# Kernel tuning notes

Measured on AMD Instinct MI355X. Metric: run time of the kernel, lower is better.

## Reference

```python
import jax, jax.numpy as jnp
import numpy as np

N_SAMPLES = 32768
WINDOW = 2048
HOP = WINDOW // 2
N_FRAMES = N_SAMPLES // HOP  # 32 resonance frames
BASE_RES = 0.5
RES_SPAN = 1.0 - BASE_RES
RES_FACTOR = 0.9
N_RES = 32
EXPR = 4
CPD = 16
N_COEFFS = WINDOW // 2 + 1  # 1025


def interpolate_last_axis(x, new_size):
    # linear interpolation along last axis (align_corners=False semantics)
    old = x.shape[-1]
    pos = (jnp.arange(new_size, dtype=jnp.float32) + 0.5) * (old / new_size) - 0.5
    pos = jnp.clip(pos, 0.0, old - 1.0)
    lo = jnp.floor(pos).astype(jnp.int32)
    hi = jnp.minimum(lo + 1, old - 1)
    w = pos - lo.astype(jnp.float32)
    return x[..., lo] * (1.0 - w) + x[..., hi] * w


def overlap_add(frames):
    # frames: (..., n_frames, window); hop = window//2; output (..., n_frames*hop)
    *lead, nf, w = frames.shape
    hop = w // 2
    a = frames[..., :hop]
    b = frames[..., hop:]
    b = jnp.concatenate([jnp.zeros_like(b[..., :1, :]), b[..., :-1, :]], axis=-2)
    return (a + b).reshape(*lead, nf * hop)


def freq_domain_transfer_function_to_resonance(window_size, decay_coeffs, n_frames, start_phase, start_mags):
    # decay_coeffs/start_phase/start_mags: (nr, expr, n_coeffs); log-space decay scan
    log_decay = jnp.log(decay_coeffs + 1e-12)[..., None, :]  # (nr, expr, 1, nc)
    shape = log_decay.shape[:-2] + (n_frames, log_decay.shape[-1])
    cum = jnp.cumsum(jnp.broadcast_to(log_decay, shape), axis=-2)  # decay^(f+1)
    mags = jnp.exp(cum) * start_mags[..., None, :]
    spec = mags * jnp.exp(1j * start_phase[..., None, :])
    frames = jnp.fft.irfft(spec, n=window_size, axis=-1)  # (nr, expr, n_frames, window)
    t = jnp.arange(window_size, dtype=jnp.float32)
    hann = 0.5 - 0.5 * jnp.cos(2.0 * jnp.pi * t / window_size)
    return overlap_add(frames * hann)  # (nr, expr, n_frames*hop)


def unit_norm(x):
    return x / (jnp.linalg.norm(x, axis=-1, keepdims=True) + 1e-8)


def fft_convolve(a, b):
    n = a.shape[-1]
    fa = jnp.fft.rfft(a, n=2 * n, axis=-1)
    fb = jnp.fft.rfft(b, n=2 * n, axis=-1)
    return jnp.fft.irfft(fa * fb, n=2 * n, axis=-1)[..., :n]


def setup_inputs() -> dict:
    key = jax.random.key(0)
    ks = jax.random.split(key, 10)
    control_signal = jax.random.normal(ks[0], (2, 4, CPD, 128), dtype=jnp.float32)
    deformations = jax.random.normal(ks[1], (2, 4, EXPR, 128), dtype=jnp.float32) * 0.1
    router = jax.random.uniform(ks[2], (CPD, N_RES), minval=-1.0, maxval=1.0)

    def init_resonance(k):
        k1, k2 = jax.random.split(k)
        res = jax.random.uniform(k1, (N_RES, N_COEFFS, 1), minval=0.01, maxval=1.0)
        deform = jax.random.uniform(k2, (1, N_COEFFS, EXPR), minval=-0.02, maxval=0.02)
        return res + deform

    amp = init_resonance(ks[3])
    phase = init_resonance(ks[4])
    decay = init_resonance(ks[5])
    gains = jax.random.uniform(ks[6], (N_RES, 1), minval=0.01, maxval=1.1)
    return {"control_signal": control_signal, "deformations": deformations,
            "router": router, "amp": amp, "phase": phase, "decay": decay, "gains": gains}


def reference(control_signal, deformations, router, amp, phase, decay, gains):
    b, e, cpd, frames = control_signal.shape
    nr = router.shape[1]
    # route control plane -> resonances: (b,e,nr,frames)
    routed = jnp.einsum('becf,cr->berf', control_signal, router)
    before_upsample = routed
    # (nr, n_coeffs, expr) -> (nr, expr, n_coeffs)
    amp_t = jnp.transpose(amp, (0, 2, 1))
    phase_t = jnp.transpose(phase, (0, 2, 1))
    decay_t = jnp.transpose(decay, (0, 2, 1))
    d_coeffs = BASE_RES + jax.nn.sigmoid(decay_t) * RES_SPAN * RES_FACTOR
    res = freq_domain_transfer_function_to_resonance(
        WINDOW, d_coeffs, N_FRAMES, jnp.tanh(phase_t) * jnp.pi, jnp.abs(amp_t))
    res = unit_norm(res)[None, None]  # (1,1,nr,expr,N)
    routed_up = interpolate_last_axis(routed[:, :, :, None, :], N_SAMPLES)  # (b,e,nr,1,N)
    noise = jax.random.uniform(jax.random.key(123), routed_up.shape, minval=-1.0, maxval=1.0)
    routed_up = routed_up * noise
    conv = fft_convolve(routed_up, res)  # (b,e,nr,expr,N)
    d = deformations.at[:, :, 0, :].add(1.0)  # base deformation favors first expressivity
    d = jax.nn.softmax(d, axis=2)[:, :, None, :, :]  # (b,e,1,expr,def_frames)
    d = interpolate_last_axis(d, N_SAMPLES)
    x = jnp.sum(d * conv, axis=-2)  # mix over expressivity -> (b,e,nr,N)
    summed = jnp.tanh(x * jnp.abs(gains).reshape(1, 1, nr, 1))
    summed = jnp.sum(summed, axis=-2, keepdims=True)  # (b,e,1,N)
    return summed, before_upsample
```

## Files before the change

### kernel.cpp

```cpp
#include <hip/hip_runtime.h>
#include <hip/hip_fp16.h>
#include <stdint.h>


#define PI_F     3.14159265358979323846f
#define TWOPI_F  6.28318530717958647692f
#define UNIT64K  (TWOPI_F/65536.0f)
#define UNIT2K   (TWOPI_F/2048.0f)
#define SCALE64K (1.0f/65536.0f)
#define SKP(i)   ((i) + 4*((i) >> 4))
#define RPW 328

__device__ __forceinline__ float2 cmul(float2 a, float2 b){
  return make_float2(a.x*b.x - a.y*b.y, a.x*b.y + a.y*b.x);
}

__device__ __forceinline__ float2 twid(uint32_t e, float unit, float sign){
  float ang = (float)e * unit;
  float sn, cn;
  __sincosf(ang, &sn, &cn);
  return make_float2(cn, sign*sn);
}

__device__ __forceinline__ uint32_t rotl32(uint32_t v, int r){
  return (v << r) | (v >> (32 - r));
}

__device__ __forceinline__ void threefry2x32(uint32_t c0, uint32_t c1,
                                             uint32_t& o0, uint32_t& o1){
  const uint32_t k0 = 0u, k1 = 123u;
  const uint32_t k2 = 0x1BD11BDAu ^ k0 ^ k1;
  const uint32_t ks[3] = {k0, k1, k2};
  uint32_t x0 = c0 + k0, x1 = c1 + k1;
#pragma unroll
  for (int i = 0; i < 5; i++){
    if ((i & 1) == 0){
      x0 += x1; x1 = rotl32(x1,13); x1 ^= x0;
      x0 += x1; x1 = rotl32(x1,15); x1 ^= x0;
      x0 += x1; x1 = rotl32(x1,26); x1 ^= x0;
      x0 += x1; x1 = rotl32(x1, 6); x1 ^= x0;
    } else {
      x0 += x1; x1 = rotl32(x1,17); x1 ^= x0;
      x0 += x1; x1 = rotl32(x1,29); x1 ^= x0;
      x0 += x1; x1 = rotl32(x1,16); x1 ^= x0;
      x0 += x1; x1 = rotl32(x1,24); x1 ^= x0;
    }
    x0 += ks[(i+1)%3];
    x1 += ks[(i+2)%3] + (uint32_t)(i+1);
  }
  o0 = x0; o1 = x1;
}

__device__ __forceinline__ float jax_noise(uint32_t p){
  uint32_t b0, b1;
  threefry2x32(0u, p, b0, b1);
  uint32_t bits = b0 ^ b1;
  float u = __uint_as_float((bits >> 9) | 0x3f800000u) - 1.0f;
  return fmaxf(-1.0f, u*2.0f - 1.0f);
}

__device__ __forceinline__ void interp128(int t, int& lo, int& hi, float& w){
  float posf = ((float)t + 0.5f) * (1.0f/256.0f) - 0.5f;
  posf = fminf(fmaxf(posf, 0.0f), 127.0f);
  lo = (int)posf;
  hi = lo + 1; if (hi > 127) hi = 127;
  w = posf - (float)lo;
}

__device__ __forceinline__ __half2 u2h(uint32_t u){
  union { uint32_t u; __half2 h; } x; x.u = u; return x.h;
}
__device__ __forceinline__ uint32_t h2u(__half2 h){
  union { uint32_t u; __half2 h; } x; x.h = h; return x.u;
}
__device__ __forceinline__ constexpr int sw4(int k){ return ((k & 3) << 2) | (k >> 2); }
__device__ __forceinline__ constexpr int br4(int x){
  return ((x & 1) << 3) | ((x & 2) << 1) | ((x & 4) >> 1) | ((x & 8) >> 3);
}

__device__ __forceinline__ void cws(float2& u, const float c, const float s){
  const float x = u.x*c - u.y*s;
  u.y = u.x*s + u.y*c;
  u.x = x;
}
__device__ __forceinline__ void cwv(float2& u, const float2 w){
  const float x = u.x*w.x - u.y*w.y;
  u.y = u.x*w.y + u.y*w.x;
  u.x = x;
}

__device__ __forceinline__ void dft4(float2& a, float2& b, float2& c, float2& d,
                                     const float sgn){
  float2 t0 = make_float2(a.x + c.x, a.y + c.y);
  float2 t1 = make_float2(a.x - c.x, a.y - c.y);
  float2 t2 = make_float2(b.x + d.x, b.y + d.y);
  float2 t3 = make_float2(b.x - d.x, b.y - d.y);
  float2 i3 = make_float2(-sgn*t3.y, sgn*t3.x);
  a = make_float2(t0.x + t2.x, t0.y + t2.y);
  c = make_float2(t0.x - t2.x, t0.y - t2.y);
  b = make_float2(t1.x + i3.x, t1.y + i3.y);
  d = make_float2(t1.x - i3.x, t1.y - i3.y);
}

#define DFT16_TW(d, sgn) do { \
  const float C1_ = 0.92387953251128674f, S1_ = 0.38268343236508978f; \
  const float C2_ = 0.70710678118654752f; \
  cws(d[5],  C1_,  (sgn)*S1_); \
  cws(d[6],  C2_,  (sgn)*C2_); \
  cws(d[7],  S1_,  (sgn)*C1_); \
  cws(d[9],  C2_,  (sgn)*C2_); \
  cws(d[10], 0.0f, (sgn)); \
  cws(d[11], -C2_, (sgn)*C2_); \
  cws(d[13], S1_,  (sgn)*C1_); \
  cws(d[14], -C2_, (sgn)*C2_); \
  cws(d[15], -C1_, -(sgn)*S1_); \
} while(0)

__device__ __forceinline__ void dft16(float2* d, const float sgn){
#pragma unroll
  for (int nb = 0; nb < 4; nb++) dft4(d[nb], d[nb+4], d[nb+8], d[nb+12], sgn);
  DFT16_TW(d, sgn);
#pragma unroll
  for (int ka = 0; ka < 4; ka++) dft4(d[4*ka], d[4*ka+1], d[4*ka+2], d[4*ka+3], sgn);
}
__device__ __forceinline__ void dft16b(float2* d, const float sgn){
#pragma unroll
  for (int nb = 0; nb < 4; nb++) dft4(d[4*nb], d[4*nb+1], d[4*nb+2], d[4*nb+3], sgn);
  DFT16_TW(d, sgn);
#pragma unroll
  for (int ka = 0; ka < 4; ka++) dft4(d[ka], d[ka+4], d[ka+8], d[ka+12], sgn);
}

__device__ __forceinline__ void pass1_fwd(__half2* buf, const float2* twl, const int t){
  const int row = t >> 4, L = t & 15;
  __half2* BR = buf + row*RPW;
  float2 d[16];
#pragma unroll
  for (int H = 0; H < 16; H++) d[H] = __half22float2(BR[L + 20*H]);
  dft16(d, -1.0f);
#pragma unroll
  for (int k1 = 0; k1 < 16; k1++){
    float2 y = d[sw4(k1)];
    cwv(y, twl[(L*k1) & 255]);
    BR[L + 20*k1] = __floats2half2_rn(y.x, y.y);
  }
}

__global__ void k_routed(const float* __restrict__ ctrl, const float* __restrict__ defm,
                         const float* __restrict__ router,
                         float* __restrict__ w_routed, float* __restrict__ w_sm,
                         float* __restrict__ out1){
  int idx = blockIdx.x*blockDim.x + threadIdx.x;
  if (idx < 32768){
    int f = idx & 127, r = (idx >> 7) & 31, be = idx >> 12;
    float acc = 0.0f;
#pragma unroll
    for (int c = 0; c < 16; c++)
      acc += ctrl[(be*16 + c)*128 + f] * router[c*32 + r];
    w_routed[idx] = acc;
    out1[idx] = acc;
  } else if (idx < 32768 + 1024){
    int j = idx - 32768;
    int f = j & 127, be = j >> 7;
    float v[4];
#pragma unroll
    for (int x = 0; x < 4; x++)
      v[x] = defm[(be*4 + x)*128 + f] + (x == 0 ? 1.0f : 0.0f);
    float mx = fmaxf(fmaxf(v[0], v[1]), fmaxf(v[2], v[3]));
    float s = 0.0f;
#pragma unroll
    for (int x = 0; x < 4; x++){ v[x] = expf(v[x] - mx); s += v[x]; }
#pragma unroll
    for (int x = 0; x < 4; x++) w_sm[(be*4 + x)*128 + f] = v[x]/s;
  }
}

__global__ void k_prep(const float* __restrict__ amp, const float* __restrict__ phase,
                       const float* __restrict__ decay, float4* __restrict__ pql){
  const int idx = blockIdx.x*256 + threadIdx.x;
  if (idx >= 131200) return;
  float a  = fabsf(amp[idx]);
  float ph = tanhf(phase[idx]) * PI_F;
  float sg = 1.0f / (1.0f + expf(-decay[idx]));
  float dc = 0.5f + 0.45f * sg;
  float L  = logf(dc + 1e-12f);
  float sn, cs;
  sincosf(ph, &sn, &cs);
  pql[idx] = make_float4(a*cs, a*sn, L, 0.0f);
}

__global__ void k_frames(const float4* __restrict__ pql, float2* __restrict__ w_fr){
  const int wg = blockIdx.x;
  const int f = wg & 31;
  const int rp = wg >> 5;
  const int p = rp & 1;
  const int r = rp >> 1;
  const int t = threadIdx.x;
  __shared__ float2 buf[2048];
  __shared__ float2 twl2[1024];

  for (int i = t; i < 1024; i += 256)
    twl2[i] = twid((uint32_t)i, UNIT2K, +1.0f);

  const float fp1 = (float)(f + 1);
  for (int k = t; k <= 1024; k += 256){
    float2 S[2];
#pragma unroll
    for (int d = 0; d < 2; d++){
      const int x = 2*p + d;
      const float4 q = pql[(r*1025 + k)*4 + x];
      const float e = __expf(q.z * fp1);
      float re = e*q.x, im = e*q.y;
      if (k == 0 || k == 1024) im = 0.0f;
      S[d] = make_float2(re, im);
    }
    buf[__brev((uint32_t)k) >> 21] =
        make_float2(S[0].x - S[1].y, S[0].y + S[1].x);
    if (k >= 1 && k <= 1023)
      buf[__brev((uint32_t)(2048 - k)) >> 21] =
          make_float2(S[0].x + S[1].y, -S[0].y + S[1].x);
  }
  __syncthreads();
  for (int s = 10; s >= 0; s--){
    const int ls = 10 - s;
    const int hl = 1 << ls;
    for (int bi = t; bi < 1024; bi += 256){
      const int g = bi >> ls, j = bi & (hl - 1);
      const int i0 = g*2*hl + j, i1 = i0 + hl;
      float2 pp = buf[i0], qq = buf[i1];
      float2 w = twl2[j << s];
      float2 v = cmul(qq, w);
      buf[i0] = make_float2(pp.x+v.x, pp.y+v.y);
      buf[i1] = make_float2(pp.x-v.x, pp.y-v.y);
    }
    __syncthreads();
  }
  float2* O = w_fr + (size_t)wg*2048;
  for (int u = t; u < 2048; u += 256){
    float hann = 0.5f - 0.5f*cosf(TWOPI_F * (float)u / 2048.0f);
    float sc = (1.0f/2048.0f) * hann;
    O[u] = make_float2(buf[u].x*sc, buf[u].y*sc);
  }
}

__global__ void k_ola(const float2* __restrict__ w_fr, float* __restrict__ w_resT,
                      float* __restrict__ w_sumsq){
  const int wg = blockIdx.x;
  const int cq = wg & 7;
  const int rp = wg >> 3;
  const int c0 = cq*32;
  const int r = rp >> 1, p = rp & 1;
  const int ch0 = r*4 + p*2;
  const int t = threadIdx.x;
  __shared__ float tx[32][129], ty[32][129];
  __shared__ float red[2][256];
  const float2* F = w_fr + (size_t)rp*32*2048;
  float acc0 = 0.0f, acc1 = 0.0f;
#pragma unroll
  for (int it = 0; it < 16; it++){
    const int idx = it*256 + t;
    const int cp = idx & 31, m = idx >> 5;
    const int n = c0 + cp + 256*m;
    const int f = n >> 10, u = n & 1023;
    float2 a = F[(size_t)f*2048 + u];
    float vx = a.x, vy = a.y;
    if (f > 0){
      float2 b = F[(size_t)(f-1)*2048 + u + 1024];
      vx += b.x; vy += b.y;
    }
    tx[cp][m] = vx; ty[cp][m] = vy;
    acc0 += vx*vx; acc1 += vy*vy;
  }
  red[0][t] = acc0; red[1][t] = acc1;
  __syncthreads();
#pragma unroll
  for (int it = 0; it < 16; it++){
    const int idx = it*256 + t;
    const int m = idx & 127, cp = idx >> 7;
    w_resT[(size_t)ch0*32768 + (size_t)(c0+cp)*128 + m]     = tx[cp][m];
    w_resT[(size_t)(ch0+1)*32768 + (size_t)(c0+cp)*128 + m] = ty[cp][m];
  }
  for (int off = 128; off > 0; off >>= 1){
    __syncthreads();
    if (t < off){ red[0][t] += red[0][t+off]; red[1][t] += red[1][t+off]; }
  }
  if (t == 0){
    atomicAdd(&w_sumsq[ch0],     red[0][0]);
    atomicAdd(&w_sumsq[ch0 + 1], red[1][0]);
  }
}

__global__ void k_norm(const float* __restrict__ w_sumsq, float* __restrict__ w_invnorm){
  const int s = threadIdx.x;
  if (s < 128) w_invnorm[s] = 1.0f/(sqrtf(w_sumsq[s]) + 1e-8f);
}

__global__ __launch_bounds__(256, 4)
void k_fwdA(const int mode, const float* __restrict__ w_resT,
            const float* __restrict__ w_invnorm,
            const float* __restrict__ w_routed,
            __half2* __restrict__ outh){
  const int wg = blockIdx.x;
  const int cq = wg & 15;
  const int sig = wg >> 4;
  const int t = threadIdx.x;
  const int cc = t >> 4;
  const int c  = cq*16 + cc;
  __shared__ alignas(16) __half2 buf[16*RPW];

  {
    const int mL = t & 15;
    float2 d[16];
    if (mode == 0){
      const int rr = sig >> 1, pq = sig & 1;
      const int ch0 = rr*4 + pq*2;
      const float inv0 = w_invnorm[ch0], inv1 = w_invnorm[ch0+1];
      const float* X0 = w_resT + (size_t)ch0*32768 + (size_t)c*128;
      const float* X1 = w_resT + (size_t)(ch0+1)*32768 + (size_t)c*128;
#pragma unroll
      for (int mH = 0; mH < 8; mH++){
        const int m = mL + 16*mH;
        d[mH] = make_float2(X0[m]*inv0, X1[m]*inv1);
      }
#pragma unroll
      for (int mH = 8; mH < 16; mH++) d[mH] = make_float2(0.0f, 0.0f);
    } else {
      const float* rp = w_routed + sig*128;
#pragma unroll
      for (int mH = 0; mH < 8; mH++){
        const int m = mL + 16*mH;
        const int n = c + 256*m;
        int lo, hi; float w;
        interp128(n, lo, hi, w);
        float rv = rp[lo]*(1.0f - w) + rp[hi]*w;
        d[mH] = make_float2(rv * jax_noise((uint32_t)sig*32768u + (uint32_t)n), 0.0f);
      }
#pragma unroll
      for (int mH = 8; mH < 16; mH++) d[mH] = make_float2(0.0f, 0.0f);
    }
    dft16(d, -1.0f);
    const float2 wstep = twid((uint32_t)(c + 256*mL) & 0xFFFFu, UNIT64K, -1.0f);
    float2 w = wstep;
    __half2* BR = buf + cc*RPW;
    BR[mL] = __floats2half2_rn(d[0].x, d[0].y);
#pragma unroll
    for (int rl = 1; rl < 16; rl++){
      float2 y = d[sw4(rl)];
      cwv(y, w);
      w = cmul(w, wstep);
      BR[20*rl + mL] = __floats2half2_rn(y.x, y.y);
    }
  }
  __syncthreads();
  {
    const int rl = t & 15;
    const __half2* BG = buf + cc*RPW + 20*rl;
    float2 v[16];
#pragma unroll
    for (int q4 = 0; q4 < 4; q4++){
      const uint4 ld = *reinterpret_cast<const uint4*>(BG + 4*q4);
      v[4*q4+0] = __half22float2(u2h(ld.x));
      v[4*q4+1] = __half22float2(u2h(ld.y));
      v[4*q4+2] = __half22float2(u2h(ld.z));
      v[4*q4+3] = __half22float2(u2h(ld.w));
    }
    dft16(v, -1.0f);
    const float2 wstep = twid((uint32_t)(16*c) & 0xFFFFu, UNIT64K, -1.0f);
    float2 w = wstep;
    __half2 y[16];
    y[0] = __floats2half2_rn(v[0].x, v[0].y);
#pragma unroll
    for (int rh = 1; rh < 16; rh++){
      float2 u = v[sw4(rh)];
      cwv(u, w);
      w = cmul(w, wstep);
      y[rh] = __floats2half2_rn(u.x, u.y);
    }
    uint4* O4 = reinterpret_cast<uint4*>(
        outh + (size_t)sig*65536 + (size_t)c*256 + 16*br4(rl));
#pragma unroll
    for (int q4 = 0; q4 < 4; q4++){
      uint4 st;
      st.x = h2u(y[br4(4*q4+0)]);
      st.y = h2u(y[br4(4*q4+1)]);
      st.z = h2u(y[br4(4*q4+2)]);
      st.w = h2u(y[br4(4*q4+3)]);
      O4[q4] = st;
    }
  }
}

__global__ __launch_bounds__(256, 4)
void k_fwdB(const __half2* __restrict__ spech, __half2* __restrict__ resp_t){
  const int wg = blockIdx.x;
  const int mq = wg & 15;
  const int sig = wg >> 4;
  const int m16 = mq*16;
  const int t = threadIdx.x;
  __shared__ alignas(16) __half2 buf[16*RPW];
  __shared__ float2 twl[256];
  twl[t] = twid((uint32_t)t << 8, UNIT64K, -1.0f);
  const __half2* base = spech + (size_t)sig*65536;
  {
    const int mm = t & 15, q = t >> 4;
    __half2* BR = buf + mm*RPW;
#pragma unroll
    for (int i = 0; i < 16; i++)
      BR[20*i + q] = base[(size_t)(16*i + q)*256 + m16 + mm];
  }
  __syncthreads();
  pass1_fwd(buf, twl, t);
  __syncthreads();
  {
    const int k1 = t >> 4, row = t & 15;
    __half2* BG = buf + row*RPW + 20*k1;
    float2 v[16];
#pragma unroll
    for (int cc = 0; cc < 4; cc++){
      const uint4 ld = *reinterpret_cast<const uint4*>(BG + 4*cc);
      v[4*cc+0] = __half22float2(u2h(ld.x));
      v[4*cc+1] = __half22float2(u2h(ld.y));
      v[4*cc+2] = __half22float2(u2h(ld.z));
      v[4*cc+3] = __half22float2(u2h(ld.w));
    }
    dft16(v, -1.0f);
    uint4* O4 = reinterpret_cast<uint4*>(resp_t + (((size_t)sig*16 + mq)*256 + t)*16);
#pragma unroll
    for (int cc = 0; cc < 4; cc++){
      uint4 st;
      st.x = h2u(__floats2half2_rn(v[4*cc+0].x, v[4*cc+0].y));
      st.y = h2u(__floats2half2_rn(v[4*cc+1].x, v[4*cc+1].y));
      st.z = h2u(__floats2half2_rn(v[4*cc+2].x, v[4*cc+2].y));
      st.w = h2u(__floats2half2_rn(v[4*cc+3].x, v[4*cc+3].y));
      O4[cc] = st;
    }
  }
}

__global__ __launch_bounds__(256, 4)
void k_conv(const __half2* __restrict__ ruspec,
            const __half2* __restrict__ resp_t,
            __half2* __restrict__ chunkbuf, const int gbase){
  const int wg = blockIdx.x;
  const int mq = wg & 15;
  const int p  = (wg >> 4) & 1;
  const int gl = wg >> 5;
  const int g = gbase + gl;
  const int r = g & 31;
  const int m16 = mq*16;
  const int t = threadIdx.x;
  __shared__ alignas(16) __half2 buf[16*RPW];
  __shared__ float2 twl[256];
  twl[t] = twid((uint32_t)t << 8, UNIT64K, -1.0f);

  {
    const uint4* A4 = reinterpret_cast<const uint4*>(
        ruspec + (size_t)g*65536 + (size_t)t*256 + m16);
    uint4 a0 = A4[0], a1 = A4[1], a2 = A4[2], a3 = A4[3];
    const int cs = SKP(t);
    uint32_t w[16];
    w[0]=a0.x; w[1]=a0.y; w[2]=a0.z; w[3]=a0.w;
    w[4]=a1.x; w[5]=a1.y; w[6]=a1.z; w[7]=a1.w;
    w[8]=a2.x; w[9]=a2.y; w[10]=a2.z; w[11]=a2.w;
    w[12]=a3.x; w[13]=a3.y; w[14]=a3.z; w[15]=a3.w;
#pragma unroll
    for (int mm = 0; mm < 16; mm++)
      buf[mm*RPW + cs] = u2h(w[mm]);
  }
  __syncthreads();
  pass1_fwd(buf, twl, t);
  __syncthreads();
  {
    const int k1 = t >> 4, row = t & 15;
    __half2* BG = buf + row*RPW + 20*k1;
    float2 v[16];
#pragma unroll
    for (int cc = 0; cc < 4; cc++){
      const uint4 ld = *reinterpret_cast<const uint4*>(BG + 4*cc);
      v[4*cc+0] = __half22float2(u2h(ld.x));
      v[4*cc+1] = __half22float2(u2h(ld.y));
      v[4*cc+2] = __half22float2(u2h(ld.z));
      v[4*cc+3] = __half22float2(u2h(ld.w));
    }
    const uint4* Bt = reinterpret_cast<const uint4*>(
        resp_t + (((size_t)(r*2 + p)*16 + mq)*256 + t)*16);
    uint4 b0 = Bt[0], b1 = Bt[1], b2 = Bt[2], b3 = Bt[3];
    dft16(v, -1.0f);
    uint32_t bw[16];
    bw[0]=b0.x; bw[1]=b0.y; bw[2]=b0.z; bw[3]=b0.w;
    bw[4]=b1.x; bw[5]=b1.y; bw[6]=b1.z; bw[7]=b1.w;
    bw[8]=b2.x; bw[9]=b2.y; bw[10]=b2.z; bw[11]=b2.w;
    bw[12]=b3.x; bw[13]=b3.y; bw[14]=b3.z; bw[15]=b3.w;
#pragma unroll
    for (int pp = 0; pp < 16; pp++){
      const float2 b = __half22float2(u2h(bw[pp]));
      const float zx = v[pp].x, zy = v[pp].y;
      v[pp] = make_float2((zx*b.x - zy*b.y)*SCALE64K,
                          (zx*b.y + zy*b.x)*SCALE64K);
    }
    dft16b(v, +1.0f);
    __half2 h[16];
#pragma unroll
    for (int n2 = 0; n2 < 16; n2++){
      float2 m = v[n2];
      const float2 w = twl[(n2*k1) & 255];
      const float x = m.x*w.x + m.y*w.y;
      m.y = -m.x*w.y + m.y*w.x;
      m.x = x;
      h[n2] = __floats2half2_rn(m.x, m.y);
    }
#pragma unroll
    for (int cc = 0; cc < 4; cc++){
      uint4 st;
      st.x = h2u(h[4*cc+0]);
      st.y = h2u(h[4*cc+1]);
      st.z = h2u(h[4*cc+2]);
      st.w = h2u(h[4*cc+3]);
      *reinterpret_cast<uint4*>(BG + 4*cc) = st;
    }
  }
  __syncthreads();
  {
    const int row = t >> 4, L = t & 15;
    __half2* BR = buf + row*RPW;
    float2 d[16];
#pragma unroll
    for (int k1 = 0; k1 < 16; k1++) d[k1] = __half22float2(BR[L + 20*k1]);
    dft16(d, +1.0f);
#pragma unroll
    for (int H = 0; H < 16; H++){
      const float2 x = d[sw4(H)];
      BR[L + 20*H] = __floats2half2_rn(x.x, x.y);
    }
  }
  __syncthreads();
  {
    uint4* O4 = reinterpret_cast<uint4*>(
        chunkbuf + (size_t)(gl*2 + p)*65536 + (size_t)t*256 + m16);
    const int cs = SKP(t);
#pragma unroll
    for (int q4 = 0; q4 < 4; q4++){
      uint4 st;
      st.x = h2u(buf[(4*q4+0)*RPW + cs]);
      st.y = h2u(buf[(4*q4+1)*RPW + cs]);
      st.z = h2u(buf[(4*q4+2)*RPW + cs]);
      st.w = h2u(buf[(4*q4+3)*RPW + cs]);
      O4[q4] = st;
    }
  }
}

__global__ __launch_bounds__(256, 4)
void k_invA_w(const __half2* __restrict__ chunkbuf, const int gbase,
              const float* __restrict__ w_sm, const float* __restrict__ gains,
              float* __restrict__ out0){
  const int wg = blockIdx.x;
  const int c8 = wg & 31;
  const int gl = wg >> 5;
  const int g = gbase + gl;
  const int r = g & 31, be = g >> 5;
  const int c0 = c8*8;
  const int t = threadIdx.x;
  __shared__ alignas(16) __half2 buf[16*RPW];
  __shared__ float sm_lds[512];
  sm_lds[t]       = w_sm[be*512 + t];
  sm_lds[256 + t] = w_sm[be*512 + 256 + t];

  const int row = t >> 4;
  const int p   = row >> 3;
  const int cc  = row & 7;
  const int c   = c0 + cc;
  {
    const int u = t & 15;
    const uint4* C4 = reinterpret_cast<const uint4*>(
        chunkbuf + (size_t)(gl*2 + p)*65536 + (size_t)c*256 + 16*br4(u));
    uint4 z0 = C4[0], z1 = C4[1], z2 = C4[2], z3 = C4[3];
    uint32_t zw[16];
    zw[0]=z0.x; zw[1]=z0.y; zw[2]=z0.z; zw[3]=z0.w;
    zw[4]=z1.x; zw[5]=z1.y; zw[6]=z1.z; zw[7]=z1.w;
    zw[8]=z2.x; zw[9]=z2.y; zw[10]=z2.z; zw[11]=z2.w;
    zw[12]=z3.x; zw[13]=z3.y; zw[14]=z3.z; zw[15]=z3.w;
    const float2 wstep = twid((uint32_t)(16*c) & 0xFFFFu, UNIT64K, +1.0f);
    float2 w = make_float2(1.0f, 0.0f);
    float2 d[16];
#pragma unroll
    for (int rh = 0; rh < 16; rh++){
      d[rh] = cmul(__half22float2(u2h(zw[br4(rh)])), w);
      w = cmul(w, wstep);
    }
    dft16(d, +1.0f);
    __half2* BR = buf + row*RPW;
#pragma unroll
    for (int mL = 0; mL < 16; mL++){
      const float2 s = d[sw4(mL)];
      BR[20*mL + u] = __floats2half2_rn(s.x, s.y);
    }
  }
  __syncthreads();
  const int mL = t & 15;
  float2 v[16];
  {
    const __half2* BG = buf + row*RPW + 20*mL;
#pragma unroll
    for (int q4 = 0; q4 < 4; q4++){
      const uint4 ld = *reinterpret_cast<const uint4*>(BG + 4*q4);
      v[4*q4+0] = __half22float2(u2h(ld.x));
      v[4*q4+1] = __half22float2(u2h(ld.y));
      v[4*q4+2] = __half22float2(u2h(ld.z));
      v[4*q4+3] = __half22float2(u2h(ld.w));
    }
  }
  __syncthreads();
  {
    const float2 wstep = twid((uint32_t)(c + 256*mL) & 0xFFFFu, UNIT64K, +1.0f);
    float2 w = wstep;
#pragma unroll
    for (int kL2 = 1; kL2 < 16; kL2++){
      v[kL2] = cmul(v[kL2], w);
      w = cmul(w, wstep);
    }
    dft16(v, +1.0f);
    __half2* BR = buf + row*RPW;
#pragma unroll
    for (int mH = 0; mH < 8; mH++){
      const float2 x = v[sw4(mH)];
      BR[mL + 20*mH] = __floats2half2_rn(x.x, x.y);
    }
  }
  __syncthreads();
  const float gv = fabsf(gains[r]);
#pragma unroll
  for (int it = 0; it < 4; it++){
    const int li = t + it*256;
    const int cc2 = li & 7, m = li >> 3;
    const int tt = c0 + cc2 + 256*m;
    int lo, hi; float w;
    interp128(tt, lo, hi, w);
    const int cell = (m & 15) + 20*(m >> 4);
    float2 z0 = __half22float2(buf[cc2*RPW + cell]);
    float2 z1 = __half22float2(buf[(8 + cc2)*RPW + cell]);
    float dw0 = sm_lds[0*128 + lo]*(1.0f - w) + sm_lds[0*128 + hi]*w;
    float dw1 = sm_lds[1*128 + lo]*(1.0f - w) + sm_lds[1*128 + hi]*w;
    float dw2 = sm_lds[2*128 + lo]*(1.0f - w) + sm_lds[2*128 + hi]*w;
    float dw3 = sm_lds[3*128 + lo]*(1.0f - w) + sm_lds[3*128 + hi]*w;
    float val = dw0*z0.x + dw1*z0.y + dw2*z1.x + dw3*z1.y;
    atomicAdd(&out0[(size_t)be*32768 + tt], tanhf(val*gv));
  }
}

extern "C" void kernel_launch(void* const* d_in, const int* in_sizes, int n_in,
                              void* d_out, int out_size, void* d_ws, size_t ws_size,
                              hipStream_t stream){
  const float* ctrl   = (const float*)d_in[0];
  const float* defm   = (const float*)d_in[1];
  const float* router = (const float*)d_in[2];
  const float* amp    = (const float*)d_in[3];
  const float* phase  = (const float*)d_in[4];
  const float* decay  = (const float*)d_in[5];
  const float* gains  = (const float*)d_in[6];
  float* out = (float*)d_out;
  float* ws  = (float*)d_ws;

  float*   w_resT    = ws;
  float*   w_routed  = ws + 4194304;
  float*   w_sm      = ws + 4227072;
  float*   w_invnorm = ws + 4231168;
  float*   w_sumsq   = ws + 4231296;
  __half2* ruspec_h  = (__half2*)(ws + 4231424);
  __half2* resp_h    = (__half2*)(ws + 21008640);
  __half2* chunk_h   = (__half2*)(ws + 25202944);
  const size_t base_f = 25202944;
  float2* w_fr       = (float2*)ruspec_h;
  __half2* resp_t    = (__half2*)w_resT;
  float4*  pql       = (float4*)resp_h;

  int G = 0;
  for (int gg = 256; gg >= 1; gg >>= 1){
    size_t need = (base_f + (size_t)gg*131072) * sizeof(float);
    if (need <= ws_size){ G = gg; break; }
  }

  hipMemsetAsync(d_out, 0, 262144*sizeof(float), stream);
  k_routed<<<132, 256, 0, stream>>>(ctrl, defm, router, w_routed, w_sm, out + 262144);
  if (G == 0) return;

  hipMemsetAsync(w_sumsq, 0, 128*sizeof(float), stream);
  k_prep<<<513, 256, 0, stream>>>(amp, phase, decay, pql);
  k_frames<<<2048, 256, 0, stream>>>(pql, w_fr);
  k_ola<<<512, 256, 0, stream>>>(w_fr, w_resT, w_sumsq);
  k_norm<<<1, 128, 0, stream>>>(w_sumsq, w_invnorm);
  k_fwdA<<<64*16, 256, 0, stream>>>(0, w_resT, w_invnorm, w_routed, resp_h);
  k_fwdB<<<64*16, 256, 0, stream>>>(resp_h, resp_t);
  k_fwdA<<<256*16, 256, 0, stream>>>(1, w_resT, w_invnorm, w_routed, ruspec_h);
  for (int gb = 0; gb < 256; gb += G){
    k_conv<<<G*32, 256, 0, stream>>>(ruspec_h, resp_t, chunk_h, gb);
    k_invA_w<<<G*32, 256, 0, stream>>>(chunk_h, gb, w_sm, gains, out);
  }
}
```

Measured before the change: 334.0 us.

## Hoist routed-signal forward FFT pass out of conv into separate kernel

The second forward FFT stage of the routed spectrum was recomputed in k_conv once for each of the two p halves. A new k_ruB kernel now computes it once per signal into a new workspace buffer, and k_conv reads the result directly before the pointwise multiply. The shared-memory twiddle table in k_conv is replaced by a per-thread recurrence of complex multiplies. This costs an extra 64 MB-scale workspace buffer, an extra global round trip, and possibly a smaller G batch if the workspace is limited; the twiddle recurrence also adds some rounding error.

```diff
diff --git a/kernel.cpp b/kernel.cpp
--- a/kernel.cpp
+++ b/kernel.cpp
@@ -438,7 +438,60 @@
 }
 
 __global__ __launch_bounds__(256, 4)
-void k_conv(const __half2* __restrict__ ruspec,
+void k_ruB(const __half2* __restrict__ ruspec, __half2* __restrict__ ruf){
+  const int wg = blockIdx.x;
+  const int mq = wg & 15;
+  const int g = wg >> 4;
+  const int m16 = mq*16;
+  const int t = threadIdx.x;
+  __shared__ alignas(16) __half2 buf[16*RPW];
+  __shared__ float2 twl[256];
+  twl[t] = twid((uint32_t)t << 8, UNIT64K, -1.0f);
+  {
+    const uint4* A4 = reinterpret_cast<const uint4*>(
+        ruspec + (size_t)g*65536 + (size_t)t*256 + m16);
+    uint4 a0 = A4[0], a1 = A4[1], a2 = A4[2], a3 = A4[3];
+    const int cs = SKP(t);
+    uint32_t w[16];
+    w[0]=a0.x; w[1]=a0.y; w[2]=a0.z; w[3]=a0.w;
+    w[4]=a1.x; w[5]=a1.y; w[6]=a1.z; w[7]=a1.w;
+    w[8]=a2.x; w[9]=a2.y; w[10]=a2.z; w[11]=a2.w;
+    w[12]=a3.x; w[13]=a3.y; w[14]=a3.z; w[15]=a3.w;
+#pragma unroll
+    for (int mm = 0; mm < 16; mm++)
+      buf[mm*RPW + cs] = u2h(w[mm]);
+  }
+  __syncthreads();
+  pass1_fwd(buf, twl, t);
+  __syncthreads();
+  {
+    const int k1 = t >> 4, row = t & 15;
+    __half2* BG = buf + row*RPW + 20*k1;
+    float2 v[16];
+#pragma unroll
+    for (int cc = 0; cc < 4; cc++){
+      const uint4 ld = *reinterpret_cast<const uint4*>(BG + 4*cc);
+      v[4*cc+0] = __half22float2(u2h(ld.x));
+      v[4*cc+1] = __half22float2(u2h(ld.y));
+      v[4*cc+2] = __half22float2(u2h(ld.z));
+      v[4*cc+3] = __half22float2(u2h(ld.w));
+    }
+    dft16(v, -1.0f);
+    uint4* O4 = reinterpret_cast<uint4*>(ruf + (((size_t)g*16 + mq)*256 + t)*16);
+#pragma unroll
+    for (int cc = 0; cc < 4; cc++){
+      uint4 st;
+      st.x = h2u(__floats2half2_rn(v[4*cc+0].x, v[4*cc+0].y));
+      st.y = h2u(__floats2half2_rn(v[4*cc+1].x, v[4*cc+1].y));
+      st.z = h2u(__floats2half2_rn(v[4*cc+2].x, v[4*cc+2].y));
+      st.w = h2u(__floats2half2_rn(v[4*cc+3].x, v[4*cc+3].y));
+      O4[cc] = st;
+    }
+  }
+}
+
+__global__ __launch_bounds__(256, 4)
+void k_conv(const __half2* __restrict__ ruf,
             const __half2* __restrict__ resp_t,
             __half2* __restrict__ chunkbuf, const int gbase){
   const int wg = blockIdx.x;
@@ -450,65 +503,44 @@
   const int m16 = mq*16;
   const int t = threadIdx.x;
   __shared__ alignas(16) __half2 buf[16*RPW];
-  __shared__ float2 twl[256];
-  twl[t] = twid((uint32_t)t << 8, UNIT64K, -1.0f);
-
-  {
-    const uint4* A4 = reinterpret_cast<const uint4*>(
-        ruspec + (size_t)g*65536 + (size_t)t*256 + m16);
-    uint4 a0 = A4[0], a1 = A4[1], a2 = A4[2], a3 = A4[3];
-    const int cs = SKP(t);
-    uint32_t w[16];
-    w[0]=a0.x; w[1]=a0.y; w[2]=a0.z; w[3]=a0.w;
-    w[4]=a1.x; w[5]=a1.y; w[6]=a1.z; w[7]=a1.w;
-    w[8]=a2.x; w[9]=a2.y; w[10]=a2.z; w[11]=a2.w;
-    w[12]=a3.x; w[13]=a3.y; w[14]=a3.z; w[15]=a3.w;
-#pragma unroll
-    for (int mm = 0; mm < 16; mm++)
-      buf[mm*RPW + cs] = u2h(w[mm]);
-  }
-  __syncthreads();
-  pass1_fwd(buf, twl, t);
-  __syncthreads();
-  {
-    const int k1 = t >> 4, row = t & 15;
-    __half2* BG = buf + row*RPW + 20*k1;
-    float2 v[16];
-#pragma unroll
-    for (int cc = 0; cc < 4; cc++){
-      const uint4 ld = *reinterpret_cast<const uint4*>(BG + 4*cc);
-      v[4*cc+0] = __half22float2(u2h(ld.x));
-      v[4*cc+1] = __half22float2(u2h(ld.y));
-      v[4*cc+2] = __half22float2(u2h(ld.z));
-      v[4*cc+3] = __half22float2(u2h(ld.w));
-    }
+
+  const int k1 = t >> 4, row = t & 15;
+  {
+    const uint4* Zt = reinterpret_cast<const uint4*>(
+        ruf + (((size_t)g*16 + mq)*256 + t)*16);
+    uint4 a0 = Zt[0], a1 = Zt[1], a2 = Zt[2], a3 = Zt[3];
     const uint4* Bt = reinterpret_cast<const uint4*>(
         resp_t + (((size_t)(r*2 + p)*16 + mq)*256 + t)*16);
     uint4 b0 = Bt[0], b1 = Bt[1], b2 = Bt[2], b3 = Bt[3];
-    dft16(v, -1.0f);
-    uint32_t bw[16];
+    uint32_t zw[16], bw[16];
+    zw[0]=a0.x; zw[1]=a0.y; zw[2]=a0.z; zw[3]=a0.w;
+    zw[4]=a1.x; zw[5]=a1.y; zw[6]=a1.z; zw[7]=a1.w;
+    zw[8]=a2.x; zw[9]=a2.y; zw[10]=a2.z; zw[11]=a2.w;
+    zw[12]=a3.x; zw[13]=a3.y; zw[14]=a3.z; zw[15]=a3.w;
     bw[0]=b0.x; bw[1]=b0.y; bw[2]=b0.z; bw[3]=b0.w;
     bw[4]=b1.x; bw[5]=b1.y; bw[6]=b1.z; bw[7]=b1.w;
     bw[8]=b2.x; bw[9]=b2.y; bw[10]=b2.z; bw[11]=b2.w;
     bw[12]=b3.x; bw[13]=b3.y; bw[14]=b3.z; bw[15]=b3.w;
+    float2 v[16];
 #pragma unroll
     for (int pp = 0; pp < 16; pp++){
+      const float2 z = __half22float2(u2h(zw[pp]));
       const float2 b = __half22float2(u2h(bw[pp]));
-      const float zx = v[pp].x, zy = v[pp].y;
-      v[pp] = make_float2((zx*b.x - zy*b.y)*SCALE64K,
-                          (zx*b.y + zy*b.x)*SCALE64K);
+      v[pp] = make_float2((z.x*b.x - z.y*b.y)*SCALE64K,
+                          (z.x*b.y + z.y*b.x)*SCALE64K);
     }
     dft16b(v, +1.0f);
+    const float2 wstep = twid((uint32_t)k1 << 8, UNIT64K, +1.0f);
+    float2 w = wstep;
     __half2 h[16];
-#pragma unroll
-    for (int n2 = 0; n2 < 16; n2++){
-      float2 m = v[n2];
-      const float2 w = twl[(n2*k1) & 255];
-      const float x = m.x*w.x + m.y*w.y;
-      m.y = -m.x*w.y + m.y*w.x;
-      m.x = x;
+    h[0] = __floats2half2_rn(v[0].x, v[0].y);
+#pragma unroll
+    for (int n2 = 1; n2 < 16; n2++){
+      float2 m = cmul(v[n2], w);
+      w = cmul(w, wstep);
       h[n2] = __floats2half2_rn(m.x, m.y);
     }
+    __half2* BG = buf + row*RPW + 20*k1;
 #pragma unroll
     for (int cc = 0; cc < 4; cc++){
       uint4 st;
@@ -521,11 +553,11 @@
   }
   __syncthreads();
   {
-    const int row = t >> 4, L = t & 15;
-    __half2* BR = buf + row*RPW;
+    const int rw = t >> 4, L = t & 15;
+    __half2* BR = buf + rw*RPW;
     float2 d[16];
 #pragma unroll
-    for (int k1 = 0; k1 < 16; k1++) d[k1] = __half22float2(BR[L + 20*k1]);
+    for (int kk = 0; kk < 16; kk++) d[kk] = __half22float2(BR[L + 20*kk]);
     dft16(d, +1.0f);
 #pragma unroll
     for (int H = 0; H < 16; H++){
@@ -668,8 +700,9 @@
   float*   w_sumsq   = ws + 4231296;
   __half2* ruspec_h  = (__half2*)(ws + 4231424);
   __half2* resp_h    = (__half2*)(ws + 21008640);
-  __half2* chunk_h   = (__half2*)(ws + 25202944);
-  const size_t base_f = 25202944;
+  __half2* ruf_h     = (__half2*)(ws + 25202944);
+  __half2* chunk_h   = (__half2*)(ws + 41980160);
+  const size_t base_f = 41980160;
   float2* w_fr       = (float2*)ruspec_h;
   __half2* resp_t    = (__half2*)w_resT;
   float4*  pql       = (float4*)resp_h;
@@ -692,8 +725,9 @@
   k_fwdA<<<64*16, 256, 0, stream>>>(0, w_resT, w_invnorm, w_routed, resp_h);
   k_fwdB<<<64*16, 256, 0, stream>>>(resp_h, resp_t);
   k_fwdA<<<256*16, 256, 0, stream>>>(1, w_resT, w_invnorm, w_routed, ruspec_h);
+  k_ruB<<<256*16, 256, 0, stream>>>(ruspec_h, ruf_h);
   for (int gb = 0; gb < 256; gb += G){
-    k_conv<<<G*32, 256, 0, stream>>>(ruspec_h, resp_t, chunk_h, gb);
+    k_conv<<<G*32, 256, 0, stream>>>(ruf_h, resp_t, chunk_h, gb);
     k_invA_w<<<G*32, 256, 0, stream>>>(chunk_h, gb, w_sm, gains, out);
   }
 }
```

New measurement: 356.9 us. +6.8%, slower.

## Share forward FFT across both response halves in k_conv workgroup

Applied to the files above, without the earlier changes.

Each k_conv workgroup now runs the input load, first forward pass and forward DFT16 once, then processes both p=0 and p=1 response halves. The forward spectrum is staged in a new 16KB shared-memory buffer in half precision and reused for the second pointwise multiply and inverse passes. This halves the ruspec reads and the forward FFT work, and launches half as many workgroups. In exchange each workgroup holds more LDS, which can reduce occupancy, and its work is more serialized.

```diff
diff --git a/kernel.cpp b/kernel.cpp
--- a/kernel.cpp
+++ b/kernel.cpp
@@ -443,13 +443,13 @@
             __half2* __restrict__ chunkbuf, const int gbase){
   const int wg = blockIdx.x;
   const int mq = wg & 15;
-  const int p  = (wg >> 4) & 1;
-  const int gl = wg >> 5;
+  const int gl = wg >> 4;
   const int g = gbase + gl;
   const int r = g & 31;
   const int m16 = mq*16;
   const int t = threadIdx.x;
   __shared__ alignas(16) __half2 buf[16*RPW];
+  __shared__ alignas(16) __half2 Fh[4096];
   __shared__ float2 twl[256];
   twl[t] = twid((uint32_t)t << 8, UNIT64K, -1.0f);
 
@@ -470,9 +470,9 @@
   __syncthreads();
   pass1_fwd(buf, twl, t);
   __syncthreads();
-  {
-    const int k1 = t >> 4, row = t & 15;
-    __half2* BG = buf + row*RPW + 20*k1;
+  const int k1 = t >> 4, row = t & 15;
+  __half2* BG = buf + row*RPW + 20*k1;
+  {
     float2 v[16];
 #pragma unroll
     for (int cc = 0; cc < 4; cc++){
@@ -482,10 +482,20 @@
       v[4*cc+2] = __half22float2(u2h(ld.z));
       v[4*cc+3] = __half22float2(u2h(ld.w));
     }
-    const uint4* Bt = reinterpret_cast<const uint4*>(
-        resp_t + (((size_t)(r*2 + p)*16 + mq)*256 + t)*16);
-    uint4 b0 = Bt[0], b1 = Bt[1], b2 = Bt[2], b3 = Bt[3];
+    const uint4* Bt0 = reinterpret_cast<const uint4*>(
+        resp_t + (((size_t)(r*2 + 0)*16 + mq)*256 + t)*16);
+    uint4 b0 = Bt0[0], b1 = Bt0[1], b2 = Bt0[2], b3 = Bt0[3];
     dft16(v, -1.0f);
+    uint4* F4 = reinterpret_cast<uint4*>(Fh + t*16);
+#pragma unroll
+    for (int cc = 0; cc < 4; cc++){
+      uint4 st;
+      st.x = h2u(__floats2half2_rn(v[4*cc+0].x, v[4*cc+0].y));
+      st.y = h2u(__floats2half2_rn(v[4*cc+1].x, v[4*cc+1].y));
+      st.z = h2u(__floats2half2_rn(v[4*cc+2].x, v[4*cc+2].y));
+      st.w = h2u(__floats2half2_rn(v[4*cc+3].x, v[4*cc+3].y));
+      F4[cc] = st;
+    }
     uint32_t bw[16];
     bw[0]=b0.x; bw[1]=b0.y; bw[2]=b0.z; bw[3]=b0.w;
     bw[4]=b1.x; bw[5]=b1.y; bw[6]=b1.z; bw[7]=b1.w;
@@ -521,11 +531,11 @@
   }
   __syncthreads();
   {
-    const int row = t >> 4, L = t & 15;
-    __half2* BR = buf + row*RPW;
+    const int rw = t >> 4, L = t & 15;
+    __half2* BR = buf + rw*RPW;
     float2 d[16];
 #pragma unroll
-    for (int k1 = 0; k1 < 16; k1++) d[k1] = __half22float2(BR[L + 20*k1]);
+    for (int kk = 0; kk < 16; kk++) d[kk] = __half22float2(BR[L + 20*kk]);
     dft16(d, +1.0f);
 #pragma unroll
     for (int H = 0; H < 16; H++){
@@ -536,7 +546,81 @@
   __syncthreads();
   {
     uint4* O4 = reinterpret_cast<uint4*>(
-        chunkbuf + (size_t)(gl*2 + p)*65536 + (size_t)t*256 + m16);
+        chunkbuf + (size_t)(gl*2 + 0)*65536 + (size_t)t*256 + m16);
+    const int cs = SKP(t);
+#pragma unroll
+    for (int q4 = 0; q4 < 4; q4++){
+      uint4 st;
+      st.x = h2u(buf[(4*q4+0)*RPW + cs]);
+      st.y = h2u(buf[(4*q4+1)*RPW + cs]);
+      st.z = h2u(buf[(4*q4+2)*RPW + cs]);
+      st.w = h2u(buf[(4*q4+3)*RPW + cs]);
+      O4[q4] = st;
+    }
+  }
+  __syncthreads();
+  {
+    const uint4* F4 = reinterpret_cast<const uint4*>(Fh + t*16);
+    uint4 a0 = F4[0], a1 = F4[1], a2 = F4[2], a3 = F4[3];
+    const uint4* Bt1 = reinterpret_cast<const uint4*>(
+        resp_t + (((size_t)(r*2 + 1)*16 + mq)*256 + t)*16);
+    uint4 b0 = Bt1[0], b1 = Bt1[1], b2 = Bt1[2], b3 = Bt1[3];
+    uint32_t zw[16], bw[16];
+    zw[0]=a0.x; zw[1]=a0.y; zw[2]=a0.z; zw[3]=a0.w;
+    zw[4]=a1.x; zw[5]=a1.y; zw[6]=a1.z; zw[7]=a1.w;
+    zw[8]=a2.x; zw[9]=a2.y; zw[10]=a2.z; zw[11]=a2.w;
+    zw[12]=a3.x; zw[13]=a3.y; zw[14]=a3.z; zw[15]=a3.w;
+    bw[0]=b0.x; bw[1]=b0.y; bw[2]=b0.z; bw[3]=b0.w;
+    bw[4]=b1.x; bw[5]=b1.y; bw[6]=b1.z; bw[7]=b1.w;
+    bw[8]=b2.x; bw[9]=b2.y; bw[10]=b2.z; bw[11]=b2.w;
+    bw[12]=b3.x; bw[13]=b3.y; bw[14]=b3.z; bw[15]=b3.w;
+    float2 v[16];
+#pragma unroll
+    for (int pp = 0; pp < 16; pp++){
+      const float2 z = __half22float2(u2h(zw[pp]));
+      const float2 b = __half22float2(u2h(bw[pp]));
+      v[pp] = make_float2((z.x*b.x - z.y*b.y)*SCALE64K,
+                          (z.x*b.y + z.y*b.x)*SCALE64K);
+    }
+    dft16b(v, +1.0f);
+    __half2 h[16];
+#pragma unroll
+    for (int n2 = 0; n2 < 16; n2++){
+      float2 m = v[n2];
+      const float2 w = twl[(n2*k1) & 255];
+      const float x = m.x*w.x + m.y*w.y;
+      m.y = -m.x*w.y + m.y*w.x;
+      m.x = x;
+      h[n2] = __floats2half2_rn(m.x, m.y);
+    }
+#pragma unroll
+    for (int cc = 0; cc < 4; cc++){
+      uint4 st;
+      st.x = h2u(h[4*cc+0]);
+      st.y = h2u(h[4*cc+1]);
+      st.z = h2u(h[4*cc+2]);
+      st.w = h2u(h[4*cc+3]);
+      *reinterpret_cast<uint4*>(BG + 4*cc) = st;
+    }
+  }
+  __syncthreads();
+  {
+    const int rw = t >> 4, L = t & 15;
+    __half2* BR = buf + rw*RPW;
+    float2 d[16];
+#pragma unroll
+    for (int kk = 0; kk < 16; kk++) d[kk] = __half22float2(BR[L + 20*kk]);
+    dft16(d, +1.0f);
+#pragma unroll
+    for (int H = 0; H < 16; H++){
+      const float2 x = d[sw4(H)];
+      BR[L + 20*H] = __floats2half2_rn(x.x, x.y);
+    }
+  }
+  __syncthreads();
+  {
+    uint4* O4 = reinterpret_cast<uint4*>(
+        chunkbuf + (size_t)(gl*2 + 1)*65536 + (size_t)t*256 + m16);
     const int cs = SKP(t);
 #pragma unroll
     for (int q4 = 0; q4 < 4; q4++){
@@ -693,7 +777,7 @@
   k_fwdB<<<64*16, 256, 0, stream>>>(resp_h, resp_t);
   k_fwdA<<<256*16, 256, 0, stream>>>(1, w_resT, w_invnorm, w_routed, ruspec_h);
   for (int gb = 0; gb < 256; gb += G){
-    k_conv<<<G*32, 256, 0, stream>>>(ruspec_h, resp_t, chunk_h, gb);
+    k_conv<<<G*16, 256, 0, stream>>>(ruspec_h, resp_t, chunk_h, gb);
     k_invA_w<<<G*32, 256, 0, stream>>>(chunk_h, gb, w_sm, gains, out);
   }
 }
```

Result: faster. 313.5 us (-6.1%).
